# Kernel tuning notes

Measured on AMD Instinct MI355X. Metric: run time of the kernel, lower is better.

The kernel has to match this reference:

```python
import jax, jax.numpy as jnp
import numpy as np
from jax import lax

B, T, N, CIN, CH, COUT, K, KS, E = 2, 16, 2048, 32, 64, 64, 3, 3, 32768


def setup_inputs() -> dict:
    key = jax.random.key(0)
    ks = jax.random.split(key, 20)
    s = 0.05
    p = lambda k, shp: s * jax.random.normal(k, shp, dtype=jnp.float32)
    return {
        "X": jax.random.normal(ks[0], (B, T, N, CIN), dtype=jnp.float32),
        "edge_index": jax.random.randint(ks[1], (2, E), 0, N),
        "edge_weight": jax.random.uniform(ks[2], (E,), dtype=jnp.float32),
        "tc1_w1": p(ks[3], (CH, CIN, 1, KS)), "tc1_b1": p(ks[4], (CH,)),
        "tc1_w2": p(ks[5], (CH, CIN, 1, KS)), "tc1_b2": p(ks[6], (CH,)),
        "tc1_w3": p(ks[7], (CH, CIN, 1, KS)), "tc1_b3": p(ks[8], (CH,)),
        "cheb_w": p(ks[9], (K, CH, CH)), "cheb_b": p(ks[10], (CH,)),
        "tc2_w1": p(ks[11], (COUT, CH, 1, KS)), "tc2_b1": p(ks[12], (COUT,)),
        "tc2_w2": p(ks[13], (COUT, CH, 1, KS)), "tc2_b2": p(ks[14], (COUT,)),
        "tc2_w3": p(ks[15], (COUT, CH, 1, KS)), "tc2_b3": p(ks[16], (COUT,)),
        "bn_gamma": jnp.ones((N,), jnp.float32),
        "bn_beta": jnp.zeros((N,), jnp.float32),
    }


def _tconv(X, w1, b1, w2, b2, w3, b3):
    # X: (B, T, N, C) -> (B, C, N, T), gated temporal conv over last axis
    x = jnp.transpose(X, (0, 3, 2, 1))
    dn = ("NCHW", "OIHW", "NCHW")
    c = lambda w, b: lax.conv_general_dilated(x, w, (1, 1), "VALID", dimension_numbers=dn) + b[None, :, None, None]
    out = jax.nn.relu(c(w1, b1) + jax.nn.sigmoid(c(w2, b2)) + c(w3, b3))
    return jnp.transpose(out, (0, 3, 2, 1))


def _cheb(x, edge_index, edge_weight, W, b):
    # ChebConv, sym normalization, lambda_max=2 -> L_hat = -D^{-1/2} A D^{-1/2}
    row, col = edge_index[0], edge_index[1]
    w = jnp.where(row == col, 0.0, edge_weight)  # get_laplacian removes self-loops
    deg = jax.ops.segment_sum(w, row, num_segments=N)
    safe = jnp.where(deg > 0, deg, 1.0)
    dis = jnp.where(deg > 0, lax.rsqrt(safe), 0.0)
    norm = -dis[row] * w * dis[col]  # (E,)

    def prop(z):  # z: (B, T, N, C)
        zm = jnp.moveaxis(z, 2, 0)                      # (N, B, T, C)
        msg = zm[col] * norm[:, None, None, None]       # (E, B, T, C)
        agg = jax.ops.segment_sum(msg, row, num_segments=N)
        return jnp.moveaxis(agg, 0, 2)

    Tx0 = x
    out = jnp.einsum("btnc,co->btno", Tx0, W[0])
    Tx1 = prop(Tx0)
    out = out + jnp.einsum("btnc,co->btno", Tx1, W[1])
    for k in range(2, K):
        Tx2 = 2.0 * prop(Tx1) - Tx0
        out = out + jnp.einsum("btnc,co->btno", Tx2, W[k])
        Tx0, Tx1 = Tx1, Tx2
    return out + b


def reference(X, edge_index, edge_weight, tc1_w1, tc1_b1, tc1_w2, tc1_b2, tc1_w3, tc1_b3,
              cheb_w, cheb_b, tc2_w1, tc2_b1, tc2_w2, tc2_b2, tc2_w3, tc2_b3,
              bn_gamma, bn_beta):
    t1 = _tconv(X, tc1_w1, tc1_b1, tc1_w2, tc1_b2, tc1_w3, tc1_b3)   # (B, T-2, N, CH)
    t2 = jax.nn.relu(_cheb(t1, edge_index, edge_weight, cheb_w, cheb_b))
    t3 = _tconv(t2, tc2_w1, tc2_b1, tc2_w2, tc2_b2, tc2_w3, tc2_b3)  # (B, T-4, N, COUT)
    t = jnp.transpose(t3, (0, 2, 1, 3))  # (B, N, T', COUT): N is BN channel axis
    mu = jnp.mean(t, axis=(0, 2, 3), keepdims=True)
    var = jnp.var(t, axis=(0, 2, 3), keepdims=True)
    t = (t - mu) * lax.rsqrt(var + 1e-5) * bn_gamma[None, :, None, None] + bn_beta[None, :, None, None]
    return jnp.transpose(t, (0, 2, 1, 3))
```

## Files before the change

kernel.cpp:

```cpp
#include <hip/hip_runtime.h>
#include <cstdint>
#include <cstddef>

typedef unsigned short ushort_t;
typedef short bf16x8 __attribute__((ext_vector_type(8)));
typedef float f32x4 __attribute__((ext_vector_type(4)));

#define N_NODES 2048
#define E_EDGES 32768

constexpr int SMALL_TOTAL = 72128;
constexpr int OFS_T1W1 = 0;
constexpr int OFS_T1B1 = 6144;
constexpr int OFS_T1W2 = 6208;
constexpr int OFS_T1B2 = 12352;
constexpr int OFS_T1W3 = 12416;
constexpr int OFS_T1B3 = 18560;
constexpr int OFS_CHW  = 18624;
constexpr int OFS_CHB  = 30912;
constexpr int OFS_T2W1 = 30976;
constexpr int OFS_T2B1 = 43264;
constexpr int OFS_T2W2 = 43328;
constexpr int OFS_T2B2 = 55616;
constexpr int OFS_T2W3 = 55680;
constexpr int OFS_T2B3 = 67968;
constexpr int OFS_GAM  = 68032;
constexpr int OFS_BET  = 70080;

__device__ __align__(16) ushort_t g_t1b [3670016];
__device__ __align__(16) ushort_t g_tx1b[3670016];
__device__ __align__(16) ushort_t g_tx2b[3670016];
__device__ __align__(16) ushort_t g_t2b [3670016];
__device__ __align__(16) float    g_t3 [3145728];
__device__ float    g_deg[N_NODES];
__device__ int      g_cnt[N_NODES];
__device__ int      g_cur[N_NODES];
__device__ __align__(8) int2 g_csrp[E_EDGES];
__device__ int      g_rowstart[N_NODES + 1];
__device__ __align__(16) ushort_t g_can[SMALL_TOTAL];
__device__ __align__(16) ushort_t g_wb1[18432];
__device__ __align__(16) ushort_t g_wb2[36864];
__device__ __align__(16) ushort_t g_wbc[12288];

__device__ __forceinline__ float bfu(ushort_t u) { return __uint_as_float(((unsigned)u) << 16); }
__device__ __forceinline__ ushort_t f2bf(float f) {
    unsigned u = __float_as_uint(f);
    u = u + 0x7fffu + ((u >> 16) & 1u);
    return (ushort_t)(u >> 16);
}
__device__ __forceinline__ float ldin(const void* p, int i, bool isbf) {
    return isbf ? bfu(((const ushort_t*)p)[i]) : ((const float*)p)[i];
}
#define BF16_ONES_PAIR 0x3F803F80u

struct SmallPtrs { const void* p[16]; };

__global__ void setup_a_kernel(const int* __restrict__ ei, const void* __restrict__ ew,
                               SmallPtrs sp, const unsigned* __restrict__ gam) {
    const bool isbf = (gam[0] == BF16_ONES_PAIR);
    int blk = blockIdx.x;
    if (blk < 128) {
        int e = blk * 256 + threadIdx.x;
        int r = ei[e];
        int c = ei[E_EDGES + e];
        float w = (r == c) ? 0.f : ldin(ew, e, isbf);
        atomicAdd(&g_deg[r], w);
        atomicAdd(&g_cnt[r], 1);
    } else {
        const int sizes[16] = {6144, 64, 6144, 64, 6144, 64, 12288, 64,
                               12288, 64, 12288, 64, 12288, 64, 2048, 2048};
        int idx = (blk - 128) * 256 + threadIdx.x;
        if (idx >= SMALL_TOTAL) return;
        int j = 0, local = idx;
        while (local >= sizes[j]) { local -= sizes[j]; ++j; }
        g_can[idx] = isbf ? ((const ushort_t*)sp.p[j])[local]
                          : f2bf(((const float*)sp.p[j])[local]);
    }
}

__global__ void scan_kernel() {
    __shared__ int part[256];
    __shared__ int pre[256];
    int t = threadIdx.x;
    int base = t * 8;
    int s = 0;
#pragma unroll
    for (int i = 0; i < 8; ++i) s += g_cnt[base + i];
    part[t] = s;
    __syncthreads();
    if (t == 0) {
        int a = 0;
        for (int i = 0; i < 256; ++i) { pre[i] = a; a += part[i]; }
    }
    __syncthreads();
    int a = pre[t];
#pragma unroll
    for (int i = 0; i < 8; ++i) { g_rowstart[base + i] = a; a += g_cnt[base + i]; }
    if (t == 255) g_rowstart[N_NODES] = a;
}

__global__ void setup_b_kernel(const int* __restrict__ ei, const void* __restrict__ ew,
                               const unsigned* __restrict__ gam) {
    int blk = blockIdx.x;
    if (blk < 128) {
        bool isbf = (gam[0] == BF16_ONES_PAIR);
        int e = blk * 256 + threadIdx.x;
        int r = ei[e];
        int c = ei[E_EDGES + e];
        float w = (r == c) ? 0.f : ldin(ew, e, isbf);
        float dr = g_deg[r], dc = g_deg[c];
        float nr = dr > 0.f ? rsqrtf(dr) : 0.f;
        float nc = dc > 0.f ? rsqrtf(dc) : 0.f;
        int pos = atomicAdd(&g_cur[r], 1);
        g_csrp[g_rowstart[r] + pos] = make_int2(c, __float_as_int(-nr * w * nc));
        return;
    }
    int idx = (blk - 128) * 256 + threadIdx.x;
    if (idx < 18432) {
        int j = idx & 7, lane = (idx >> 3) & 63, kk = (idx >> 9) % 3;
        int nt = (idx / 1536) & 3, set = idx / 6144;
        int o = nt * 16 + (lane & 15);
        int k = kk * 32 + (lane >> 4) * 8 + j;
        int ci = k & 31, ks = k >> 5;
        int base = (set == 0) ? OFS_T1W1 : (set == 1) ? OFS_T1W2 : OFS_T1W3;
        g_wb1[idx] = g_can[base + o * 96 + ci * 3 + ks];
    } else if (idx < 18432 + 36864) {
        int t = idx - 18432;
        int j = t & 7, lane = (t >> 3) & 63, kk = (t >> 9) % 6;
        int nt = (t / 3072) & 3, set = t / 12288;
        int o = nt * 16 + (lane & 15);
        int k = kk * 32 + (lane >> 4) * 8 + j;
        int ci = k & 63, ks = k >> 6;
        int base = (set == 0) ? OFS_T2W1 : (set == 1) ? OFS_T2W2 : OFS_T2W3;
        g_wb2[t] = g_can[base + o * 192 + ci * 3 + ks];
    } else {
        int t = idx - 18432 - 36864;
        int j = t & 7, lane = (t >> 3) & 63, kk = (t >> 9) % 6;
        int nt = t / 3072;
        int o = nt * 16 + (lane & 15);
        int k = kk * 32 + (lane >> 4) * 8 + j;
        int sec = k >> 6, c = k & 63;
        g_wbc[t] = g_can[OFS_CHW + sec * 4096 + c * 64 + o];
    }
}

template <int LAYER>
__global__ __launch_bounds__(256) void tconv_mfma_kernel(const void* __restrict__ Xraw,
                                                         const unsigned* __restrict__ gam) {
    constexpr int CIN_  = (LAYER == 1) ? 32 : 64;
    constexpr int T_in  = (LAYER == 1) ? 16 : 14;
    constexpr int T_out = (LAYER == 1) ? 14 : 12;
    constexpr int KST   = (CIN_ * 3) / 32;
    constexpr int PADK  = (LAYER == 1) ? 104 : 200;
    constexpr int OB1 = (LAYER == 1) ? OFS_T1B1 : OFS_T2B1;
    constexpr int OB2 = (LAYER == 1) ? OFS_T1B2 : OFS_T2B2;
    constexpr int OB3 = (LAYER == 1) ? OFS_T1B3 : OFS_T2B3;

    __shared__ ushort_t xs[64 * PADK];

    const int tid = threadIdx.x;
    const int lane = tid & 63;
    const int wv = tid >> 6;
    const int m0 = blockIdx.x * 64;
    const int n0 = m0 & (N_NODES - 1);
    const int s  = m0 >> 11;
    const int b  = s / T_out;
    const int t  = s - b * T_out;

    if constexpr (LAYER == 1) {
        if (blockIdx.x < 8) {
            int z = blockIdx.x * 256 + tid;
            g_deg[z] = 0.f; g_cnt[z] = 0; g_cur[z] = 0;
        }
    }

#pragma unroll
    for (int ks = 0; ks < 3; ++ks) {
        if constexpr (LAYER == 1) {
            const bool isbf = (gam[0] == BF16_ONES_PAIR);
            const size_t elo = ((size_t)(b * T_in + t + ks) * N_NODES + n0) * 32;
            if (isbf) {
                const ushort4* src = (const ushort4*)((const ushort_t*)Xraw + elo);
                for (int i = tid; i < 512; i += 256) {
                    ushort4 v = src[i];
                    int row = i >> 3, c4 = i & 7;
                    *(ushort4*)&xs[row * PADK + ks * 32 + c4 * 4] = v;
                }
            } else {
                const float4* src = (const float4*)((const float*)Xraw + elo);
                for (int i = tid; i < 512; i += 256) {
                    float4 f = src[i];
                    ushort4 v;
                    v.x = f2bf(f.x); v.y = f2bf(f.y); v.z = f2bf(f.z); v.w = f2bf(f.w);
                    int row = i >> 3, c4 = i & 7;
                    *(ushort4*)&xs[row * PADK + ks * 32 + c4 * 4] = v;
                }
            }
        } else {
            const ushort4* src = (const ushort4*)(g_t2b +
                ((size_t)(b * T_in + t + ks) * N_NODES + n0) * 64);
            for (int i = tid; i < 1024; i += 256) {
                ushort4 v = src[i];
                int row = i >> 4, c4 = i & 15;
                *(ushort4*)&xs[row * PADK + ks * 64 + c4 * 4] = v;
            }
        }
    }
    __syncthreads();

    const ushort_t* WB = (LAYER == 1) ? g_wb1 : g_wb2;
    f32x4 acc[3][4];
#pragma unroll
    for (int st = 0; st < 3; ++st)
#pragma unroll
        for (int nt = 0; nt < 4; ++nt) acc[st][nt] = (f32x4){0.f, 0.f, 0.f, 0.f};

    const int arow = wv * 16 + (lane & 15);
    const int kofs = (lane >> 4) * 8;
#pragma unroll
    for (int kk = 0; kk < KST; ++kk) {
        bf16x8 av = *(const bf16x8*)&xs[arow * PADK + kk * 32 + kofs];
#pragma unroll
        for (int st = 0; st < 3; ++st)
#pragma unroll
            for (int nt = 0; nt < 4; ++nt) {
                bf16x8 bv = ((const bf16x8*)WB)[((st * 4 + nt) * KST + kk) * 64 + lane];
                acc[st][nt] = __builtin_amdgcn_mfma_f32_16x16x32_bf16(av, bv, acc[st][nt], 0, 0, 0);
            }
    }

    const int col = lane & 15;
    const int quad = lane >> 4;
#pragma unroll
    for (int nt = 0; nt < 4; ++nt) {
        int o = nt * 16 + col;
        float b1 = bfu(g_can[OB1 + o]);
        float b2 = bfu(g_can[OB2 + o]);
        float b3 = bfu(g_can[OB3 + o]);
#pragma unroll
        for (int reg = 0; reg < 4; ++reg) {
            int m = m0 + wv * 16 + quad * 4 + reg;
            float q = acc[1][nt][reg] + b2;
            float v = (acc[0][nt][reg] + b1) + 1.f / (1.f + expf(-q)) + (acc[2][nt][reg] + b3);
            v = v > 0.f ? v : 0.f;
            if constexpr (LAYER == 1) g_t1b[(size_t)m * 64 + o] = f2bf(v);
            else                      g_t3 [(size_t)m * 64 + o] = v;
        }
    }
}

template <int MODE>
__global__ __launch_bounds__(256) void prop_kernel() {
    const ushort_t* __restrict__ src = (MODE == 0) ? g_t1b : g_tx1b;
    ushort_t* __restrict__ dst = (MODE == 0) ? g_tx1b : g_tx2b;
    const int n = blockIdx.x;
    const int c = threadIdx.x & 63;
    const int sg = threadIdx.x >> 6;
    const int beg = g_rowstart[n], end = g_rowstart[n + 1];
    const int s0 = sg * 7;

    float acc[7];
#pragma unroll
    for (int j = 0; j < 7; ++j) acc[j] = 0.f;

    int e = beg;
    for (; e + 2 <= end; e += 2) {
        int2 p0 = g_csrp[e];
        int2 p1 = g_csrp[e + 1];
        float w0 = __int_as_float(p0.y);
        float w1 = __int_as_float(p1.y);
        size_t b0 = ((size_t)p0.x << 6) + c;
        size_t b1 = ((size_t)p1.x << 6) + c;
#pragma unroll
        for (int j = 0; j < 7; ++j) {
            size_t so = (size_t)(s0 + j) * (N_NODES * 64);
            float v0 = bfu(src[so + b0]);
            float v1 = bfu(src[so + b1]);
            acc[j] = fmaf(w1, v1, fmaf(w0, v0, acc[j]));
        }
    }
    if (e < end) {
        int2 p0 = g_csrp[e];
        float w0 = __int_as_float(p0.y);
        size_t b0 = ((size_t)p0.x << 6) + c;
#pragma unroll
        for (int j = 0; j < 7; ++j)
            acc[j] = fmaf(w0, bfu(src[(size_t)(s0 + j) * (N_NODES * 64) + b0]), acc[j]);
    }

#pragma unroll
    for (int j = 0; j < 7; ++j) {
        size_t off = ((size_t)(s0 + j) * N_NODES + n) * 64 + c;
        if constexpr (MODE == 0) dst[off] = f2bf(acc[j]);
        else                     dst[off] = f2bf(2.f * acc[j] - bfu(g_t1b[off]));
    }
}

__global__ __launch_bounds__(256) void cheb_mfma_kernel() {
    constexpr int PADK = 200;
    __shared__ ushort_t xs[64 * PADK];

    const int tid = threadIdx.x;
    const int lane = tid & 63;
    const int wv = tid >> 6;
    const int m0 = blockIdx.x * 64;

#pragma unroll
    for (int sec = 0; sec < 3; ++sec) {
        const ushort_t* sp = (sec == 0) ? g_t1b : (sec == 1) ? g_tx1b : g_tx2b;
        const ushort4* src = (const ushort4*)(sp + (size_t)m0 * 64);
        for (int i = tid; i < 1024; i += 256) {
            ushort4 v = src[i];
            int row = i >> 4, c4 = i & 15;
            *(ushort4*)&xs[row * PADK + sec * 64 + c4 * 4] = v;
        }
    }
    __syncthreads();

    f32x4 acc[4];
#pragma unroll
    for (int nt = 0; nt < 4; ++nt) acc[nt] = (f32x4){0.f, 0.f, 0.f, 0.f};

    const int arow = wv * 16 + (lane & 15);
    const int kofs = (lane >> 4) * 8;
#pragma unroll
    for (int kk = 0; kk < 6; ++kk) {
        bf16x8 av = *(const bf16x8*)&xs[arow * PADK + kk * 32 + kofs];
#pragma unroll
        for (int nt = 0; nt < 4; ++nt) {
            bf16x8 bv = ((const bf16x8*)g_wbc)[(nt * 6 + kk) * 64 + lane];
            acc[nt] = __builtin_amdgcn_mfma_f32_16x16x32_bf16(av, bv, acc[nt], 0, 0, 0);
        }
    }

    const int col = lane & 15;
    const int quad = lane >> 4;
#pragma unroll
    for (int nt = 0; nt < 4; ++nt) {
        int o = nt * 16 + col;
        float bias = bfu(g_can[OFS_CHB + o]);
#pragma unroll
        for (int reg = 0; reg < 4; ++reg) {
            int m = m0 + wv * 16 + quad * 4 + reg;
            float v = acc[nt][reg] + bias;
            g_t2b[(size_t)m * 64 + o] = f2bf(v > 0.f ? v : 0.f);
        }
    }
}

__global__ __launch_bounds__(256) void bn_fused_kernel(void* __restrict__ outp,
                                                       const unsigned* __restrict__ gam) {
    int n = blockIdx.x;
    int tid = threadIdx.x;
    int c = tid & 63;
    int sg = tid >> 6;
    float vals[6];
    float s1 = 0.f, s2 = 0.f;
    int k = 0;
    for (int s = sg; s < 24; s += 4, ++k) {
        float v = g_t3[((size_t)(s * N_NODES + n)) * 64 + c];
        vals[k] = v;
        s1 += v;
        s2 += v * v;
    }
    __shared__ float r1[256], r2[256];
    __shared__ float sc_s, sh_s;
    r1[tid] = s1;
    r2[tid] = s2;
    __syncthreads();
    for (int st = 128; st > 0; st >>= 1) {
        if (tid < st) { r1[tid] += r1[tid + st]; r2[tid] += r2[tid + st]; }
        __syncthreads();
    }
    if (tid == 0) {
        const float inv = 1.f / 1536.f;
        float mean = r1[0] * inv;
        float var  = r2[0] * inv - mean * mean;
        float rstd = rsqrtf(var + 1e-5f);
        float g = bfu(g_can[OFS_GAM + n]), be = bfu(g_can[OFS_BET + n]);
        sc_s = rstd * g;
        sh_s = be - mean * rstd * g;
    }
    __syncthreads();
    float sc = sc_s, sh = sh_s;
    bool isbf = (gam[0] == BF16_ONES_PAIR);
    k = 0;
    for (int s = sg; s < 24; s += 4, ++k) {
        size_t off = ((size_t)(s * N_NODES + n)) * 64 + c;
        float r = vals[k] * sc + sh;
        if (isbf) ((ushort_t*)outp)[off] = f2bf(r);
        else      ((float*)outp)[off] = r;
    }
}

extern "C" void kernel_launch(void* const* d_in, const int* in_sizes, int n_in,
                              void* d_out, int out_size, void* d_ws, size_t ws_size,
                              hipStream_t stream) {
    const void* X = d_in[0];
    const int* ei = (const int*)d_in[1];
    const void* ew = d_in[2];
    const unsigned* gam = (const unsigned*)d_in[17];

    SmallPtrs sp;
    for (int i = 0; i < 16; ++i) sp.p[i] = d_in[3 + i];

    setup_a_kernel<<<410, 256, 0, stream>>>(ei, ew, sp, gam);
    scan_kernel<<<1, 256, 0, stream>>>();
    setup_b_kernel<<<392, 256, 0, stream>>>(ei, ew, gam);

    tconv_mfma_kernel<1><<<896, 256, 0, stream>>>(X, gam);

    prop_kernel<0><<<N_NODES, 256, 0, stream>>>();
    prop_kernel<1><<<N_NODES, 256, 0, stream>>>();
    cheb_mfma_kernel<<<896, 256, 0, stream>>>();

    tconv_mfma_kernel<2><<<768, 256, 0, stream>>>(X, gam);

    bn_fused_kernel<<<N_NODES, 256, 0, stream>>>(d_out, gam);
}
```

Measured before the change: 186.7 us.

## Double the M tile in the tconv and cheb MFMA kernels to reuse B fragments

The gated temporal conv and Chebyshev MFMA kernels now handle 128 rows per block instead of 64. Each wave computes two 16-row M subtiles, so every weight fragment fetched from global memory feeds two MFMAs, and the grid sizes are halved to match. The aim is to cut repeated weight loads and per-block overhead. In exchange, LDS per block and accumulator registers double, and the grids shrink to a few hundred blocks, which lowers occupancy and may leave some compute units underused.

```diff
diff --git a/kernel.cpp b/kernel.cpp
--- a/kernel.cpp
+++ b/kernel.cpp
@@ -156,12 +156,12 @@
     constexpr int OB2 = (LAYER == 1) ? OFS_T1B2 : OFS_T2B2;
     constexpr int OB3 = (LAYER == 1) ? OFS_T1B3 : OFS_T2B3;
 
-    __shared__ ushort_t xs[64 * PADK];
+    __shared__ ushort_t xs[128 * PADK];
 
     const int tid = threadIdx.x;
     const int lane = tid & 63;
     const int wv = tid >> 6;
-    const int m0 = blockIdx.x * 64;
+    const int m0 = blockIdx.x * 128;
     const int n0 = m0 & (N_NODES - 1);
     const int s  = m0 >> 11;
     const int b  = s / T_out;
@@ -181,14 +181,14 @@
             const size_t elo = ((size_t)(b * T_in + t + ks) * N_NODES + n0) * 32;
             if (isbf) {
                 const ushort4* src = (const ushort4*)((const ushort_t*)Xraw + elo);
-                for (int i = tid; i < 512; i += 256) {
+                for (int i = tid; i < 1024; i += 256) {
                     ushort4 v = src[i];
                     int row = i >> 3, c4 = i & 7;
                     *(ushort4*)&xs[row * PADK + ks * 32 + c4 * 4] = v;
                 }
             } else {
                 const float4* src = (const float4*)((const float*)Xraw + elo);
-                for (int i = tid; i < 512; i += 256) {
+                for (int i = tid; i < 1024; i += 256) {
                     float4 f = src[i];
                     ushort4 v;
                     v.x = f2bf(f.x); v.y = f2bf(f.y); v.z = f2bf(f.z); v.w = f2bf(f.w);
@@ -199,7 +199,7 @@
         } else {
             const ushort4* src = (const ushort4*)(g_t2b +
                 ((size_t)(b * T_in + t + ks) * N_NODES + n0) * 64);
-            for (int i = tid; i < 1024; i += 256) {
+            for (int i = tid; i < 2048; i += 256) {
                 ushort4 v = src[i];
                 int row = i >> 4, c4 = i & 15;
                 *(ushort4*)&xs[row * PADK + ks * 64 + c4 * 4] = v;
@@ -209,44 +209,50 @@
     __syncthreads();
 
     const ushort_t* WB = (LAYER == 1) ? g_wb1 : g_wb2;
-    f32x4 acc[3][4];
-#pragma unroll
-    for (int st = 0; st < 3; ++st)
-#pragma unroll
-        for (int nt = 0; nt < 4; ++nt) acc[st][nt] = (f32x4){0.f, 0.f, 0.f, 0.f};
-
-    const int arow = wv * 16 + (lane & 15);
+    f32x4 acc[2][3][4];
+#pragma unroll
+    for (int mt = 0; mt < 2; ++mt)
+#pragma unroll
+        for (int st = 0; st < 3; ++st)
+#pragma unroll
+            for (int nt = 0; nt < 4; ++nt) acc[mt][st][nt] = (f32x4){0.f, 0.f, 0.f, 0.f};
+
+    const int arow = wv * 32 + (lane & 15);
     const int kofs = (lane >> 4) * 8;
 #pragma unroll
     for (int kk = 0; kk < KST; ++kk) {
-        bf16x8 av = *(const bf16x8*)&xs[arow * PADK + kk * 32 + kofs];
+        bf16x8 av0 = *(const bf16x8*)&xs[arow * PADK + kk * 32 + kofs];
+        bf16x8 av1 = *(const bf16x8*)&xs[(arow + 16) * PADK + kk * 32 + kofs];
 #pragma unroll
         for (int st = 0; st < 3; ++st)
 #pragma unroll
             for (int nt = 0; nt < 4; ++nt) {
                 bf16x8 bv = ((const bf16x8*)WB)[((st * 4 + nt) * KST + kk) * 64 + lane];
-                acc[st][nt] = __builtin_amdgcn_mfma_f32_16x16x32_bf16(av, bv, acc[st][nt], 0, 0, 0);
+                acc[0][st][nt] = __builtin_amdgcn_mfma_f32_16x16x32_bf16(av0, bv, acc[0][st][nt], 0, 0, 0);
+                acc[1][st][nt] = __builtin_amdgcn_mfma_f32_16x16x32_bf16(av1, bv, acc[1][st][nt], 0, 0, 0);
             }
     }
 
     const int col = lane & 15;
     const int quad = lane >> 4;
 #pragma unroll
-    for (int nt = 0; nt < 4; ++nt) {
-        int o = nt * 16 + col;
-        float b1 = bfu(g_can[OB1 + o]);
-        float b2 = bfu(g_can[OB2 + o]);
-        float b3 = bfu(g_can[OB3 + o]);
-#pragma unroll
-        for (int reg = 0; reg < 4; ++reg) {
-            int m = m0 + wv * 16 + quad * 4 + reg;
-            float q = acc[1][nt][reg] + b2;
-            float v = (acc[0][nt][reg] + b1) + 1.f / (1.f + expf(-q)) + (acc[2][nt][reg] + b3);
-            v = v > 0.f ? v : 0.f;
-            if constexpr (LAYER == 1) g_t1b[(size_t)m * 64 + o] = f2bf(v);
-            else                      g_t3 [(size_t)m * 64 + o] = v;
-        }
-    }
+    for (int mt = 0; mt < 2; ++mt)
+#pragma unroll
+        for (int nt = 0; nt < 4; ++nt) {
+            int o = nt * 16 + col;
+            float b1 = bfu(g_can[OB1 + o]);
+            float b2 = bfu(g_can[OB2 + o]);
+            float b3 = bfu(g_can[OB3 + o]);
+#pragma unroll
+            for (int reg = 0; reg < 4; ++reg) {
+                int m = m0 + wv * 32 + mt * 16 + quad * 4 + reg;
+                float q = acc[mt][1][nt][reg] + b2;
+                float v = (acc[mt][0][nt][reg] + b1) + 1.f / (1.f + expf(-q)) + (acc[mt][2][nt][reg] + b3);
+                v = v > 0.f ? v : 0.f;
+                if constexpr (LAYER == 1) g_t1b[(size_t)m * 64 + o] = f2bf(v);
+                else                      g_t3 [(size_t)m * 64 + o] = v;
+            }
+        }
 }
 
 template <int MODE>
@@ -298,18 +304,18 @@
 
 __global__ __launch_bounds__(256) void cheb_mfma_kernel() {
     constexpr int PADK = 200;
-    __shared__ ushort_t xs[64 * PADK];
+    __shared__ ushort_t xs[128 * PADK];
 
     const int tid = threadIdx.x;
     const int lane = tid & 63;
     const int wv = tid >> 6;
-    const int m0 = blockIdx.x * 64;
+    const int m0 = blockIdx.x * 128;
 
 #pragma unroll
     for (int sec = 0; sec < 3; ++sec) {
         const ushort_t* sp = (sec == 0) ? g_t1b : (sec == 1) ? g_tx1b : g_tx2b;
         const ushort4* src = (const ushort4*)(sp + (size_t)m0 * 64);
-        for (int i = tid; i < 1024; i += 256) {
+        for (int i = tid; i < 2048; i += 256) {
             ushort4 v = src[i];
             int row = i >> 4, c4 = i & 15;
             *(ushort4*)&xs[row * PADK + sec * 64 + c4 * 4] = v;
@@ -317,35 +323,41 @@
     }
     __syncthreads();
 
-    f32x4 acc[4];
-#pragma unroll
-    for (int nt = 0; nt < 4; ++nt) acc[nt] = (f32x4){0.f, 0.f, 0.f, 0.f};
-
-    const int arow = wv * 16 + (lane & 15);
+    f32x4 acc[2][4];
+#pragma unroll
+    for (int mt = 0; mt < 2; ++mt)
+#pragma unroll
+        for (int nt = 0; nt < 4; ++nt) acc[mt][nt] = (f32x4){0.f, 0.f, 0.f, 0.f};
+
+    const int arow = wv * 32 + (lane & 15);
     const int kofs = (lane >> 4) * 8;
 #pragma unroll
     for (int kk = 0; kk < 6; ++kk) {
-        bf16x8 av = *(const bf16x8*)&xs[arow * PADK + kk * 32 + kofs];
+        bf16x8 av0 = *(const bf16x8*)&xs[arow * PADK + kk * 32 + kofs];
+        bf16x8 av1 = *(const bf16x8*)&xs[(arow + 16) * PADK + kk * 32 + kofs];
 #pragma unroll
         for (int nt = 0; nt < 4; ++nt) {
             bf16x8 bv = ((const bf16x8*)g_wbc)[(nt * 6 + kk) * 64 + lane];
-            acc[nt] = __builtin_amdgcn_mfma_f32_16x16x32_bf16(av, bv, acc[nt], 0, 0, 0);
+            acc[0][nt] = __builtin_amdgcn_mfma_f32_16x16x32_bf16(av0, bv, acc[0][nt], 0, 0, 0);
+            acc[1][nt] = __builtin_amdgcn_mfma_f32_16x16x32_bf16(av1, bv, acc[1][nt], 0, 0, 0);
         }
     }
 
     const int col = lane & 15;
     const int quad = lane >> 4;
 #pragma unroll
-    for (int nt = 0; nt < 4; ++nt) {
-        int o = nt * 16 + col;
-        float bias = bfu(g_can[OFS_CHB + o]);
-#pragma unroll
-        for (int reg = 0; reg < 4; ++reg) {
-            int m = m0 + wv * 16 + quad * 4 + reg;
-            float v = acc[nt][reg] + bias;
-            g_t2b[(size_t)m * 64 + o] = f2bf(v > 0.f ? v : 0.f);
-        }
-    }
+    for (int mt = 0; mt < 2; ++mt)
+#pragma unroll
+        for (int nt = 0; nt < 4; ++nt) {
+            int o = nt * 16 + col;
+            float bias = bfu(g_can[OFS_CHB + o]);
+#pragma unroll
+            for (int reg = 0; reg < 4; ++reg) {
+                int m = m0 + wv * 32 + mt * 16 + quad * 4 + reg;
+                float v = acc[mt][nt][reg] + bias;
+                g_t2b[(size_t)m * 64 + o] = f2bf(v > 0.f ? v : 0.f);
+            }
+        }
 }
 
 __global__ __launch_bounds__(256) void bn_fused_kernel(void* __restrict__ outp,
@@ -408,13 +420,13 @@
     scan_kernel<<<1, 256, 0, stream>>>();
     setup_b_kernel<<<392, 256, 0, stream>>>(ei, ew, gam);
 
-    tconv_mfma_kernel<1><<<896, 256, 0, stream>>>(X, gam);
+    tconv_mfma_kernel<1><<<448, 256, 0, stream>>>(X, gam);
 
     prop_kernel<0><<<N_NODES, 256, 0, stream>>>();
     prop_kernel<1><<<N_NODES, 256, 0, stream>>>();
-    cheb_mfma_kernel<<<896, 256, 0, stream>>>();
-
-    tconv_mfma_kernel<2><<<768, 256, 0, stream>>>(X, gam);
+    cheb_mfma_kernel<<<448, 256, 0, stream>>>();
+
+    tconv_mfma_kernel<2><<<384, 256, 0, stream>>>(X, gam);
 
     bn_fused_kernel<<<N_NODES, 256, 0, stream>>>(d_out, gam);
 }
```

New measurement: 199.3 us. 1.07x slower.
